# Kernel optimization log

Hardware: AMD Instinct MI355X
Metric: run time of the kernel (lower is better)

Reference implementation:

```python
import jax, jax.numpy as jnp
import numpy as np

H_DIM = 128; N_HEADS = 4; D_K = 32; W_INP = 300
N_DOC = 32000; N_TOPIC = 800; N_WORD = 80000; B = 16
VOCAB = 15000; N_TOPIC_EMB = 50
SQRT_DK = float(np.sqrt(D_K))


def setup_inputs() -> dict:
    key = jax.random.key(0)
    ks = iter(jax.random.split(key, 64))
    def nrm(shape, s=0.05):
        return jax.random.normal(next(ks), shape, dtype=jnp.float32) * s
    def ridx(shape, hi):
        return jax.random.randint(next(ks), shape, 0, hi, dtype=jnp.int32)
    inp = {
        'word_embeds': nrm((VOCAB, W_INP), 0.1),
        'topic_embeds': nrm((N_TOPIC_EMB, H_DIM), 0.1),
        'KW': nrm((2, 3, H_DIM, H_DIM)), 'Kb': nrm((2, 3, H_DIM)),
        'QW': nrm((2, 3, H_DIM, H_DIM)), 'Qb': nrm((2, 3, H_DIM)),
        'VW': nrm((2, 3, H_DIM, H_DIM)), 'Vb': nrm((2, 3, H_DIM)),
        'AW': nrm((2, 3, H_DIM, H_DIM)), 'Ab': nrm((2, 3, H_DIM)),
        'rel_att': nrm((2, 5, N_HEADS, D_K, D_K), 0.1),
        'rel_msg': nrm((2, 5, N_HEADS, D_K, D_K), 0.1),
        'rel_pri': jnp.ones((2, 5, N_HEADS), jnp.float32),
        'skip': jnp.ones((2, 3), jnp.float32),
        'adapt_w': nrm((W_INP, H_DIM)), 'adapt_b': nrm((H_DIM,)),
        'out_w': nrm((H_DIM, 1)), 'out_b': nrm((1,)),
        'y_data': jax.random.uniform(next(ks), (B,), dtype=jnp.float32),
        'word_ids': ridx((N_WORD,), VOCAB),
        'topic_ids': ridx((N_TOPIC,), N_TOPIC_EMB),
        'doc_gid': jnp.sort(ridx((N_DOC,), B)),
        'td_src': ridx((80000,), N_TOPIC), 'td_dst': ridx((80000,), N_DOC),
        'tt_src': ridx((20000,), N_TOPIC), 'tt_dst': ridx((20000,), N_TOPIC),
        'wd_src': ridx((250000,), N_WORD), 'wd_dst': ridx((250000,), N_DOC),
        'wt_src': ridx((100000,), N_WORD), 'wt_dst': ridx((100000,), N_TOPIC),
        'ww_src': ridx((400000,), N_WORD), 'ww_dst': ridx((400000,), N_WORD),
    }
    return inp


def _seg_attn(att, val, dst, n):
    # per-dst-node softmax over incoming edges (per head), then weighted scatter-sum
    m = jax.ops.segment_max(att, dst, num_segments=n)          # [n, H]
    m = jnp.where(jnp.isfinite(m), m, 0.0)                     # empty mailboxes -> 0
    e = jnp.exp(att - m[dst])                                  # [E, H]
    s = jax.ops.segment_sum(e, dst, num_segments=n)            # [n, H]
    w = e / jnp.where(s[dst] > 0, s[dst], 1.0)                 # [E, H]
    return jax.ops.segment_sum(w[:, :, None] * val, dst, num_segments=n)  # [n, H, dk]


def _proj(h, W, b):
    return (h @ W + b).reshape(-1, N_HEADS, D_K)


def _forward(word_embeds, topic_embeds, KW, Kb, QW, Qb, VW, Vb, AW, Ab,
             rel_att, rel_msg, rel_pri, skip, adapt_w, adapt_b, out_w, out_b,
             y_data, word_ids, topic_ids, doc_gid,
             td_src, td_dst, tt_src, tt_dst, wd_src, wd_dst,
             wt_src, wt_dst, ww_src, ww_dst):
    # node-type ids: doc=0, topic=1, word=2; etype ids: td=0 tt=1 wd=2 wt=3 ww=4
    hw = jnp.tanh(word_embeds[word_ids] @ adapt_w + adapt_b)   # [Nw, H_DIM]
    ht = topic_embeds[topic_ids]                               # [Nt, H_DIM]
    hd = jnp.zeros((N_DOC, H_DIM), dtype=word_embeds.dtype)

    def layer(hd, ht, hw, li):
        q_d = _proj(hd, QW[li, 0], Qb[li, 0])
        q_t = _proj(ht, QW[li, 1], Qb[li, 1])
        q_w = _proj(hw, QW[li, 2], Qb[li, 2])
        k_t = _proj(ht, KW[li, 1], Kb[li, 1]); v_t = _proj(ht, VW[li, 1], Vb[li, 1])
        k_w = _proj(hw, KW[li, 2], Kb[li, 2]); v_w = _proj(hw, VW[li, 2], Vb[li, 2])

        def et(k, v, q, src, dst, r, n_dst):
            ke = jnp.einsum('ehd,hdf->ehf', k[src], rel_att[li, r])
            att = (q[dst] * ke).sum(-1) * rel_pri[li, r] / SQRT_DK   # [E, H]
            val = jnp.einsum('ehd,hdf->ehf', v[src], rel_msg[li, r])
            return _seg_attn(att, val, dst, n_dst)

        # cross_reducer='mean' over etypes targeting each node type
        t_d = (et(k_t, v_t, q_d, td_src, td_dst, 0, N_DOC) +
               et(k_w, v_w, q_d, wd_src, wd_dst, 2, N_DOC)) * 0.5
        t_t = (et(k_t, v_t, q_t, tt_src, tt_dst, 1, N_TOPIC) +
               et(k_w, v_w, q_t, wt_src, wt_dst, 3, N_TOPIC)) * 0.5
        t_w = et(k_w, v_w, q_w, ww_src, ww_dst, 4, N_WORD)

        def comb(t, h, nid):
            a = jax.nn.sigmoid(skip[li, nid])
            tr = t.reshape(-1, H_DIM) @ AW[li, nid] + Ab[li, nid]
            return tr * a + h * (1.0 - a)

        return comb(t_d, hd, 0), comb(t_t, ht, 1), comb(t_w, hw, 2)

    for li in range(2):
        hd, ht, hw = layer(hd, ht, hw, li)

    g = jax.ops.segment_max(hd, doc_gid, num_segments=B)       # dgl.max_nodes over docs
    logits = (g @ out_w + out_b).reshape(-1)                   # [B]
    loss = jnp.mean(-(y_data * jax.nn.log_sigmoid(logits) +
                      (1.0 - y_data) * jax.nn.log_sigmoid(-logits)))
    return loss, jax.nn.sigmoid(logits)[:, None]


def reference(word_embeds, topic_embeds, KW, Kb, QW, Qb, VW, Vb, AW, Ab,
              rel_att, rel_msg, rel_pri, skip, adapt_w, adapt_b, out_w, out_b,
              y_data, word_ids, topic_ids, doc_gid,
              td_src, td_dst, tt_src, tt_dst, wd_src, wd_dst,
              wt_src, wt_dst, ww_src, ww_dst):
    return _forward(word_embeds, topic_embeds, KW, Kb, QW, Qb, VW, Vb, AW, Ab,
                    rel_att, rel_msg, rel_pri, skip, adapt_w, adapt_b, out_w, out_b,
                    y_data, word_ids, topic_ids, doc_gid,
                    td_src, td_dst, tt_src, tt_dst, wd_src, wd_dst,
                    wt_src, wt_dst, ww_src, ww_dst)
```

## Files before the change

kernel.cpp:

```cpp
#include <hip/hip_runtime.h>
#include <cstdint>
#include <cstddef>

#define H_DIM 128
#define N_DOC 32000
#define N_TOPIC 800
#define N_WORD 80000
#define BATCH 16
#define VOCAB 15000
#define NODES_ALL 145600
#define EDGES_ALL 850000
#define NBLK_SCAN 143
#define N4_SCAN 36400
#define LDSW 136

typedef short bf16x8 __attribute__((ext_vector_type(8)));
typedef float f32x4 __attribute__((ext_vector_type(4)));
typedef float f32x2 __attribute__((ext_vector_type(2)));
typedef unsigned short u16;
typedef unsigned char u8;

static __device__ __forceinline__ u16 f2bf(float x) {
  unsigned u = __float_as_uint(x);
  u += 0x7fffu + ((u >> 16) & 1u);
// ... 60 lines not shown
      W = AW + ((size_t)li * 3 + nid) * 16384; b = Ab + ((size_t)li * 3 + nid) * 128;
      R = rel_msg + ((size_t)li * 5 + r) * 4096;
      scale = (r == 4) ? 1.f : 0.5f;
    }
  }
  u16* obl = (wid == 0) ? bl_arena : bl_arena + 40960 + (size_t)(wid - 1) * 16384;
  float* obias = bias_arena + wid * 128;

  const int nelem = KS * 512;
  for (int e = threadIdx.x; e < nelem; e += 256) {
    const int s = e >> 9, rem = e & 511, l = rem >> 3, jj = rem & 7;
    const int k = s * 32 + ((l >> 4) << 3) + jj;
    const int nn = t * 16 + (l & 15);
    float v = 0.f;
    if (k < Kreal) {
      if (fold == 0) v = W[(size_t)k * 128 + nn];
      else if (fold == 1) {
        const int h = nn >> 5, d = nn & 31;
        const float* Wr = W + (size_t)k * 128 + h * 32;
        const float* Rh = R + h * 1024;
        for (int f = 0; f < 32; ++f) v += Wr[f] * Rh[d * 32 + f];
      } else {
        const int h = k >> 5, dd = k & 31;
        const float* Rh = R + h * 1024 + dd * 32;
        const float* Wc = W + (size_t)h * 32 * 128 + nn;
        float sa = 0.f;
        for (int f = 0; f < 32; ++f) sa += Rh[f] * Wc[(size_t)f * 128];
        v = sa * scale;
      }
    }
    obl[(size_t)(t * KS + s) * 512 + rem] = f2bf(v);
  }
  if (t == 0 && threadIdx.x < 128) {
    const int nn = threadIdx.x;
    float v = 0.f;
    if (fold != 1) v = b[nn];
    else {
      const int h = nn >> 5, d = nn & 31;
      const float* Rh = R + h * 1024;
      for (int f = 0; f < 32; ++f) v += b[h * 32 + f] * Rh[d * 32 + f];
    }
    obias[nn] = v;
  }
}

static __device__ __forceinline__ void kv_write_half(
    const u16* lds16, int rr, int cs, u8* kv, size_t m, int vhalf)
{
  u8* Cp = kv + m * 256 + (cs >> 3) * 16 + (vhalf ? 8 : 0);
  #pragma unroll
  for (int q2 = 0; q2 < 4; ++q2) {
    uint4 ld = *reinterpret_cast<const uint4*>(&lds16[rr * LDSW + cs + q2 * 8]);
    int t0 = __builtin_amdgcn_cvt_pk_fp8_f32(b2f(ld.x & 0xffffu), b2f(ld.x >> 16), 0, false);
    unsigned w0 = (unsigned)__builtin_amdgcn_cvt_pk_fp8_f32(b2f(ld.y & 0xffffu), b2f(ld.y >> 16), t0, true);
    int t1 = __builtin_amdgcn_cvt_pk_fp8_f32(b2f(ld.z & 0xffffu), b2f(ld.z >> 16), 0, false);
    unsigned w1 = (unsigned)__builtin_amdgcn_cvt_pk_fp8_f32(b2f(ld.w & 0xffffu), b2f(ld.w >> 16), t1, true);
    *reinterpret_cast<uint2*>(Cp + q2 * 16) = make_uint2(w0, w1);
  }
}

static __device__ __forceinline__ void bf16_write_row(
    const u16* lds16, int rr, int cs, u16* C, size_t m)
{
  u16* Cp = C + m * 128 + cs;
  #pragma unroll
  for (int q2 = 0; q2 < 4; ++q2)
    *reinterpret_cast<uint4*>(Cp + q2 * 8) =
        *reinterpret_cast<const uint4*>(&lds16[rr * LDSW + cs + q2 * 8]);
}

#define GEMM_ACC(AV, BLP)                                                        \
  {                                                                              \
    const u16* Bp = (BLP) + (size_t)lane * 8;                                    \
    _Pragma("unroll")                                                            \
    for (int s = 0; s < 4; ++s) {                                                \
      _Pragma("unroll")                                                          \
      for (int t = 0; t < 8; ++t) {                                              \
        bf16x8 bfr = *reinterpret_cast<const bf16x8*>(Bp + (size_t)(t * 4 + s) * 512); \
        acc[t] = __builtin_amdgcn_mfma_f32_16x16x32_bf16(AV[s], bfr, acc[t], 0, 0, 0); \
      }                                                                          \
    }                                                                            \
  }

#define ACC_TO_LDS(BIAS)                                                         \
  {                                                                              \
    _Pragma("unroll")                                                            \
    for (int t = 0; t < 8; ++t) {                                                \
      const int col = t * 16 + (lane & 15);                                      \
      const float bb = (BIAS)[col];                                              \
      const int mr = w * 16 + g * 4;                                             \
      _Pragma("unroll")                                                          \
      for (int j = 0; j < 4; ++j)                                                \
        lds16[(mr + j) * LDSW + col] = f2bf(acc[t][j] + bb);                     \
    }                                                                            \
  }

static __device__ __forceinline__ float lds_qc_dot(
    const u16* lds16, int rr, int cs, const float* __restrict__ qc)
{
  float dot = 0.f;
  #pragma unroll
  for (int q2 = 0; q2 < 4; ++q2) {
    uint4 ld = *reinterpret_cast<const uint4*>(&lds16[rr * LDSW + cs + q2 * 8]);
    float4 qa = *reinterpret_cast<const float4*>(&qc[cs + q2 * 8]);
    float4 qb = *reinterpret_cast<const float4*>(&qc[cs + q2 * 8 + 4]);
    dot += b2f(ld.x & 0xffffu) * qa.x + b2f(ld.x >> 16) * qa.y
         + b2f(ld.y & 0xffffu) * qa.z + b2f(ld.y >> 16) * qa.w
         + b2f(ld.z & 0xffffu) * qb.x + b2f(ld.z >> 16) * qb.y
         + b2f(ld.w & 0xffffu) * qb.z + b2f(ld.w >> 16) * qb.w;
  }
  return dot;
}

static __device__ __forceinline__ void vp_write(
    const u16* lds16, int rr, int cs, float u_keep, u8* vp, size_t m)
{
  unsigned wpk[8];
  #pragma unroll
  for (int q2 = 0; q2 < 4; ++q2) {
    uint4 ld = *reinterpret_cast<const uint4*>(&lds16[rr * LDSW + cs + q2 * 8]);
    int t0 = __builtin_amdgcn_cvt_pk_fp8_f32(u_keep * b2f(ld.x & 0xffffu), u_keep * b2f(ld.x >> 16), 0, false);
    wpk[2 * q2] = (unsigned)__builtin_amdgcn_cvt_pk_fp8_f32(u_keep * b2f(ld.y & 0xffffu), u_keep * b2f(ld.y >> 16), t0, true);
    int t1 = __builtin_amdgcn_cvt_pk_fp8_f32(u_keep * b2f(ld.z & 0xffffu), u_keep * b2f(ld.z >> 16), 0, false);
    wpk[2 * q2 + 1] = (unsigned)__builtin_amdgcn_cvt_pk_fp8_f32(u_keep * b2f(ld.w & 0xffffu), u_keep * b2f(ld.w >> 16), t1, true);
  }
  *reinterpret_cast<uint4*>(vp + m * 128 + cs)      = make_uint4(wpk[0], wpk[1], wpk[2], wpk[3]);
  *reinterpret_cast<uint4*>(vp + m * 128 + cs + 16) = make_uint4(wpk[4], wpk[5], wpk[6], wpk[7]);
}

__global__ __launch_bounds__(256) void adapt_l0w_kernel(
    const u16* __restrict__ wtab, const int* __restrict__ word_ids,
    const u16* __restrict__ BLa, const float* __restrict__ ba,
    const u16* __restrict__ BLk, const float* __restrict__ bk,
    const u16* __restrict__ BLv, const float* __restrict__ bv,
    const u16* __restrict__ BLq, const float* __restrict__ bq,
    const float* __restrict__ qc, const float* __restrict__ priw,
    u16* __restrict__ hw, u8* __restrict__ kv, u8* __restrict__ vp,
    float* __restrict__ uf, u16* __restrict__ qout, int n)
{
  __shared__ u16 lds16[64 * LDSW];
  const int tid = threadIdx.x, lane = tid & 63, w = tid >> 6;
  int rl = blockIdx.x * 64 + w * 16 + (lane & 15);
  if (rl >= n) rl = n - 1;
  const int row = word_ids[rl];
  const int g = lane >> 4;

  bf16x8 a10[10];
  const u16* Ap = wtab + (size_t)row * 320 + g * 8;
  #pragma unroll
  for (int s = 0; s < 10; ++s) a10[s] = *reinterpret_cast<const bf16x8*>(Ap + s * 32);

  const int rr = w * 16 + (lane >> 2), cs = (lane & 3) * 32;
  const int m = blockIdx.x * 64 + rr;

  f32x4 acc[8];
  #pragma unroll
  for (int t = 0; t < 8; ++t) acc[t] = (f32x4)0.f;
  {
    const u16* Bp = BLa + (size_t)lane * 8;
    #pragma unroll
    for (int s = 0; s < 10; ++s) {
      #pragma unroll
      for (int t = 0; t < 8; ++t) {
        bf16x8 bfr = *reinterpret_cast<const bf16x8*>(Bp + (size_t)(t * 10 + s) * 512);
        acc[t] = __builtin_amdgcn_mfma_f32_16x16x32_bf16(a10[s], bfr, acc[t], 0, 0, 0);
      }
    }
  }
  #pragma unroll
  for (int t = 0; t < 8; ++t) {
    const int col = t * 16 + (lane & 15);
    const float bb = ba[col];
    const int mr = w * 16 + g * 4;
    #pragma unroll
    for (int j = 0; j < 4; ++j)
      lds16[(mr + j) * LDSW + col] = f2bf(tanhf(acc[t][j] + bb));
  }
  if (m < n) bf16_write_row(lds16, rr, cs, hw, m);
  bf16x8 an[4];
  {
    const int rloc = w * 16 + (lane & 15);
    #pragma unroll
    for (int s = 0; s < 4; ++s)
      an[s] = *reinterpret_cast<const bf16x8*>(&lds16[rloc * LDSW + s * 32 + g * 8]);
  }

  #pragma unroll
  for (int t = 0; t < 8; ++t) acc[t] = (f32x4)0.f;
  GEMM_ACC(an, BLk)
  ACC_TO_LDS(bk)
  float u_keep = 0.f;
  if (m < n) {
    kv_write_half(lds16, rr, cs, kv, m, 0);
    float dot = lds_qc_dot(lds16, rr, cs, qc);
    u_keep = __expf(dot * (priw[cs >> 5] * 0.17677669529663687f));
    uf[m * 4 + (cs >> 5)] = u_keep;
  }
  #pragma unroll
  for (int t = 0; t < 8; ++t) acc[t] = (f32x4)0.f;
  GEMM_ACC(an, BLv)
  ACC_TO_LDS(bv)
  if (m < n) {
    kv_write_half(lds16, rr, cs, kv, m, 1);
    vp_write(lds16, rr, cs, u_keep, vp, m);
  }
  #pragma unroll
  for (int t = 0; t < 8; ++t) acc[t] = (f32x4)0.f;
  GEMM_ACC(an, BLq)
  ACC_TO_LDS(bq)
  if (m < n) bf16_write_row(lds16, rr, cs, qout, m);
}

__global__ __launch_bounds__(256) void gemm_kv_kernel(
    const u16* __restrict__ A,
    const u16* __restrict__ BLk, const float* __restrict__ bk,
    const u16* __restrict__ BLv, const float* __restrict__ bv,
    u8* __restrict__ kv, int n)
{
  __shared__ u16 lds16[64 * LDSW];
  const int tid = threadIdx.x, lane = tid & 63, w = tid >> 6;
  int rl = blockIdx.x * 64 + w * 16 + (lane & 15);
  if (rl >= n) rl = n - 1;
  const int g = lane >> 4;
  bf16x8 a[4];
  const u16* Ap = A + (size_t)rl * 128 + g * 8;
  #pragma unroll
  for (int s = 0; s < 4; ++s) a[s] = *reinterpret_cast<const bf16x8*>(Ap + s * 32);
  const int rr = w * 16 + (lane >> 2), cs = (lane & 3) * 32;
  const int m = blockIdx.x * 64 + rr;

  f32x4 acc[8];
  #pragma unroll
  for (int t = 0; t < 8; ++t) acc[t] = (f32x4)0.f;
  GEMM_ACC(a, BLk)
  ACC_TO_LDS(bk)
  if (m < n) kv_write_half(lds16, rr, cs, kv, m, 0);

  #pragma unroll
  for (int t = 0; t < 8; ++t) acc[t] = (f32x4)0.f;
  GEMM_ACC(a, BLv)
  ACC_TO_LDS(bv)
  if (m < n) kv_write_half(lds16, rr, cs, kv, m, 1);
}

__global__ __launch_bounds__(256) void gemmN_l0t_kernel(
    const u16* __restrict__ A,
    const u16* __restrict__ BLk, const float* __restrict__ bk,
    const u16* __restrict__ BLv, const float* __restrict__ bv,
    const u16* __restrict__ BLq0, const float* __restrict__ bq0,
    const u16* __restrict__ BLq1, const float* __restrict__ bq1,
    const float* __restrict__ qc, const float* __restrict__ prit,
    u8* __restrict__ kv, u8* __restrict__ vp, float* __restrict__ uf,
    u16* __restrict__ q0, u16* __restrict__ q1, int n)
{
  __shared__ u16 lds16[64 * LDSW];
  const int tid = threadIdx.x, lane = tid & 63, w = tid >> 6;
  int rl = blockIdx.x * 64 + w * 16 + (lane & 15);
  if (rl >= n) rl = n - 1;
  const int g = lane >> 4;
  bf16x8 a[4];
  const u16* Ap = A + (size_t)rl * 128 + g * 8;
  #pragma unroll
  for (int s = 0; s < 4; ++s) a[s] = *reinterpret_cast<const bf16x8*>(Ap + s * 32);
  const int rr = w * 16 + (lane >> 2), cs = (lane & 3) * 32;
  const int m = blockIdx.x * 64 + rr;

  f32x4 acc[8];
  #pragma unroll
  for (int t = 0; t < 8; ++t) acc[t] = (f32x4)0.f;
  GEMM_ACC(a, BLk)
  ACC_TO_LDS(bk)
  float u_keep = 0.f;
  if (m < n) {
    kv_write_half(lds16, rr, cs, kv, m, 0);
    float dot = lds_qc_dot(lds16, rr, cs, qc);
    u_keep = __expf(dot * (prit[cs >> 5] * 0.17677669529663687f));
    uf[m * 4 + (cs >> 5)] = u_keep;
  }
  #pragma unroll
  for (int t = 0; t < 8; ++t) acc[t] = (f32x4)0.f;
  GEMM_ACC(a, BLv)
  ACC_TO_LDS(bv)
  if (m < n) {
    kv_write_half(lds16, rr, cs, kv, m, 1);
    vp_write(lds16, rr, cs, u_keep, vp, m);
  }
  #pragma unroll
  for (int t = 0; t < 8; ++t) acc[t] = (f32x4)0.f;
  GEMM_ACC(a, BLq0)
  ACC_TO_LDS(bq0)
  if (m < n) bf16_write_row(lds16, rr, cs, q0, m);

  #pragma unroll
  for (int t = 0; t < 8; ++t) acc[t] = (f32x4)0.f;
  GEMM_ACC(a, BLq1)
  ACC_TO_LDS(bq1)
  if (m < n) bf16_write_row(lds16, rr, cs, q1, m);
}

template<int KS>
__global__ __launch_bounds__(256) void gemm2_kernel(
    const u16* __restrict__ A2, const u16* __restrict__ BL0, const u16* __restrict__ BL1,
    const float* __restrict__ bias, u16* __restrict__ C,
    const float* __restrict__ skipp, int n)
{
  __shared__ u16 lds16[64 * LDSW];
  const int tid = threadIdx.x, lane = tid & 63, w = tid >> 6;
  int rl = blockIdx.x * 64 + w * 16 + (lane & 15);
  if (rl >= n) rl = n - 1;
  const int g = lane >> 4;

  bf16x8 a0[KS], a1[KS];
  const u16* Ap = A2 + (size_t)rl * 256 + g * 8;
  #pragma unroll
  for (int s = 0; s < KS; ++s) {
    a0[s] = *reinterpret_cast<const bf16x8*>(Ap + s * 32);
    a1[s] = *reinterpret_cast<const bf16x8*>(Ap + 128 + s * 32);
  }
  f32x4 acc[8];
  #pragma unroll
  for (int t = 0; t < 8; ++t) acc[t] = (f32x4)0.f;
  const u16* Bp0 = BL0 + (size_t)lane * 8;
  const u16* Bp1 = BL1 + (size_t)lane * 8;
  #pragma unroll
  for (int s = 0; s < KS; ++s) {
    #pragma unroll
    for (int t = 0; t < 8; ++t) {
      bf16x8 b0 = *reinterpret_cast<const bf16x8*>(Bp0 + (size_t)(t * KS + s) * 512);
      acc[t] = __builtin_amdgcn_mfma_f32_16x16x32_bf16(a0[s], b0, acc[t], 0, 0, 0);
      bf16x8 b1 = *reinterpret_cast<const bf16x8*>(Bp1 + (size_t)(t * KS + s) * 512);
      acc[t] = __builtin_amdgcn_mfma_f32_16x16x32_bf16(a1[s], b1, acc[t], 0, 0, 0);
    }
  }
  ACC_TO_LDS(bias)
  const int rr = w * 16 + (lane >> 2), cs = (lane & 3) * 32;
  const int m = blockIdx.x * 64 + rr;
  if (m < n) {
    const float aa = 1.f / (1.f + __expf(-skipp[0]));
    #pragma unroll
    for (int q2 = 0; q2 < 4; ++q2) {
      uint4 pr = *reinterpret_cast<const uint4*>(&lds16[rr * LDSW + cs + q2 * 8]);
      uint4 blv = *reinterpret_cast<const uint4*>(C + (size_t)m * 128 + cs + q2 * 8);
      uint4 st;
      st.x = blend2(pr.x, blv.x, aa);
      st.y = blend2(pr.y, blv.y, aa);
      st.z = blend2(pr.z, blv.z, aa);
      st.w = blend2(pr.w, blv.w, aa);
      *reinterpret_cast<uint4*>(C + (size_t)m * 128 + cs + q2 * 8) = st;
    }
  }
}

__global__ __launch_bounds__(256) void comb_dq_kernel(
    const u16* __restrict__ A2, const u16* __restrict__ BL0, const u16* __restrict__ BL1,
    const float* __restrict__ bias, const float* __restrict__ skipp,
    const u16* __restrict__ BLq0, const float* __restrict__ bq0,
    const u16* __restrict__ BLq1, const float* __restrict__ bq1,
    u16* __restrict__ hd, u16* __restrict__ q0, u16* __restrict__ q1, int n)
{
  __shared__ u16 lds16[64 * LDSW];
  const int tid = threadIdx.x, lane = tid & 63, w = tid >> 6;
  int rl = blockIdx.x * 64 + w * 16 + (lane & 15);
  if (rl >= n) rl = n - 1;
  const int g = lane >> 4;

  bf16x8 a0[4], a1[4];
  const u16* Ap = A2 + (size_t)rl * 256 + g * 8;
  #pragma unroll
  for (int s = 0; s < 4; ++s) {
    a0[s] = *reinterpret_cast<const bf16x8*>(Ap + s * 32);
    a1[s] = *reinterpret_cast<const bf16x8*>(Ap + 128 + s * 32);
  }
  f32x4 acc[8];
  #pragma unroll
  for (int t = 0; t < 8; ++t) acc[t] = (f32x4)0.f;
  {
    const u16* Bp0 = BL0 + (size_t)lane * 8;
    const u16* Bp1 = BL1 + (size_t)lane * 8;
    #pragma unroll
    for (int s = 0; s < 4; ++s) {
      #pragma unroll
      for (int t = 0; t < 8; ++t) {
        bf16x8 b0 = *reinterpret_cast<const bf16x8*>(Bp0 + (size_t)(t * 4 + s) * 512);
        acc[t] = __builtin_amdgcn_mfma_f32_16x16x32_bf16(a0[s], b0, acc[t], 0, 0, 0);
        bf16x8 b1 = *reinterpret_cast<const bf16x8*>(Bp1 + (size_t)(t * 4 + s) * 512);
        acc[t] = __builtin_amdgcn_mfma_f32_16x16x32_bf16(a1[s], b1, acc[t], 0, 0, 0);
      }
    }
  }
  const float aa = 1.f / (1.f + __expf(-skipp[0]));
  #pragma unroll
  for (int t = 0; t < 8; ++t) {
    const int col = t * 16 + (lane & 15);
    const float bb = bias[col];
    const int mr = w * 16 + g * 4;
    #pragma unroll
    for (int j = 0; j < 4; ++j)
      lds16[(mr + j) * LDSW + col] = f2bf((acc[t][j] + bb) * aa);
  }
  const int rr = w * 16 + (lane >> 2), cs = (lane & 3) * 32;
  const int m = blockIdx.x * 64 + rr;
  if (m < n) bf16_write_row(lds16, rr, cs, hd, m);
  bf16x8 an[4];
  {
    const int rloc = w * 16 + (lane & 15);
    #pragma unroll
    for (int s = 0; s < 4; ++s)
      an[s] = *reinterpret_cast<const bf16x8*>(&lds16[rloc * LDSW + s * 32 + g * 8]);
  }
  #pragma unroll
  for (int t = 0; t < 8; ++t) acc[t] = (f32x4)0.f;
  GEMM_ACC(an, BLq0)
  ACC_TO_LDS(bq0)
  if (m < n) bf16_write_row(lds16, rr, cs, q0, m);
  #pragma unroll
  for (int t = 0; t < 8; ++t) acc[t] = (f32x4)0.f;
  GEMM_ACC(an, BLq1)
  ACC_TO_LDS(bq1)
  if (m < n) bf16_write_row(lds16, rr, cs, q1, m);
}

__global__ __launch_bounds__(256) void comb_kv_kernel(
    const u16* __restrict__ Aw, const u16* __restrict__ hwold,
    const u16* __restrict__ BLc, const float* __restrict__ bc,
    const u16* __restrict__ BLk, const float* __restrict__ bk,
    const u16* __restrict__ BLv, const float* __restrict__ bv,
    const float* __restrict__ skipp, u8* __restrict__ kv, int n)
{
  __shared__ u16 lds16[64 * LDSW];
  const int tid = threadIdx.x, lane = tid & 63, w = tid >> 6;
  int rl = blockIdx.x * 64 + w * 16 + (lane & 15);
  if (rl >= n) rl = n - 1;
  const int g = lane >> 4;

  bf16x8 a[4];
  const u16* Ap = Aw + (size_t)rl * 128 + g * 8;
  #pragma unroll
  for (int s = 0; s < 4; ++s) a[s] = *reinterpret_cast<const bf16x8*>(Ap + s * 32);

  f32x4 acc[8];
  #pragma unroll
  for (int t = 0; t < 8; ++t) acc[t] = (f32x4)0.f;
  GEMM_ACC(a, BLc)
  ACC_TO_LDS(bc)
  const int rr = w * 16 + (lane >> 2), cs = (lane & 3) * 32;
  const int m = blockIdx.x * 64 + rr;
  if (m < n) {
    const float aa = 1.f / (1.f + __expf(-skipp[0]));
    #pragma unroll
    for (int q2 = 0; q2 < 4; ++q2) {
      uint4 pr = *reinterpret_cast<const uint4*>(&lds16[rr * LDSW + cs + q2 * 8]);
      uint4 blv = *reinterpret_cast<const uint4*>(hwold + (size_t)m * 128 + cs + q2 * 8);
      uint4 st;
      st.x = blend2(pr.x, blv.x, aa);
      st.y = blend2(pr.y, blv.y, aa);
      st.z = blend2(pr.z, blv.z, aa);
      st.w = blend2(pr.w, blv.w, aa);
      *reinterpret_cast<uint4*>(&lds16[rr * LDSW + cs + q2 * 8]) = st;
    }
  }
  bf16x8 an[4];
  {
    const int rloc = w * 16 + (lane & 15);
    #pragma unroll
    for (int s = 0; s < 4; ++s)
      an[s] = *reinterpret_cast<const bf16x8*>(&lds16[rloc * LDSW + s * 32 + g * 8]);
  }
  #pragma unroll
  for (int t = 0; t < 8; ++t) acc[t] = (f32x4)0.f;
  GEMM_ACC(an, BLk)
  ACC_TO_LDS(bk)
  if (m < n) kv_write_half(lds16, rr, cs, kv, m, 0);
  #pragma unroll
  for (int t = 0; t < 8; ++t) acc[t] = (f32x4)0.f;
  GEMM_ACC(an, BLv)
  ACC_TO_LDS(bv)
  if (m < n) kv_write_half(lds16, rr, cs, kv, m, 1);
}

__global__ void conv_wtab_kernel(const float* __restrict__ we, u16* __restrict__ wt) {
  int i = blockIdx.x * 256 + threadIdx.x;
  if (i < VOCAB * 320) {
    int r = i / 320, c = i - r * 320;
    wt[i] = (c < 300) ? f2bf(we[(size_t)r * 300 + c]) : (u16)0;
  }
}

__global__ void gather_topic_kernel(const float* __restrict__ emb, const int* __restrict__ ids,
                                    u16* __restrict__ out) {
  int i = blockIdx.x * 256 + threadIdx.x;
  if (i < N_TOPIC * 128) {
    int node = i >> 7, c = i & 127;
    out[i] = f2bf(emb[(size_t)ids[node] * 128 + c]);
  }
}

__global__ void count_rank_kernel(const int* __restrict__ td, const int* __restrict__ wd,
                                  const int* __restrict__ tt, const int* __restrict__ wt,
                                  const int* __restrict__ ww, int* cnt, int* __restrict__ rank) {
  int i = blockIdx.x * 256 + threadIdx.x;
  if (i >= EDGES_ALL) return;
  int b;
  if (i < 80000)       b = td[i];
  else if (i < 330000) b = 32000 + wd[i - 80000];
  else if (i < 350000) b = 64000 + tt[i - 330000];
  else if (i < 450000) b = 64800 + wt[i - 350000];
  else                 b = 65600 + ww[i - 450000];
  rank[i] = atomicAdd(&cnt[b], 1);
}

__global__ void fill_rank_kernel(const int* __restrict__ td_s, const int* __restrict__ td_d,
                                 const int* __restrict__ wd_s, const int* __restrict__ wd_d,
                                 const int* __restrict__ tt_s, const int* __restrict__ tt_d,
                                 const int* __restrict__ wt_s, const int* __restrict__ wt_d,
                                 const int* __restrict__ ww_s, const int* __restrict__ ww_d,
                                 const int* __restrict__ offs, const int* __restrict__ rank,
                                 int* __restrict__ csrc) {
  int i = blockIdx.x * 256 + threadIdx.x;
  if (i >= EDGES_ALL) return;
  int b, s;
  if (i < 80000)       { b = td_d[i];                  s = td_s[i]; }
  else if (i < 330000) { b = 32000 + wd_d[i - 80000];  s = wd_s[i - 80000]; }
  else if (i < 350000) { b = 64000 + tt_d[i - 330000]; s = tt_s[i - 330000]; }
  else if (i < 450000) { b = 64800 + wt_d[i - 350000]; s = wt_s[i - 350000]; }
  else                 { b = 65600 + ww_d[i - 450000]; s = ww_s[i - 450000]; }
  csrc[offs[b] + rank[i]] = s;
}

__global__ __launch_bounds__(256) void scanA_kernel(const int* __restrict__ cnt, int* __restrict__ bsum) {
  const int tid = threadIdx.x, lane = tid & 63, wv = tid >> 6;
  const int i4 = blockIdx.x * 256 + tid;
  int4 v = make_int4(0, 0, 0, 0);
  if (i4 < N4_SCAN) v = reinterpret_cast<const int4*>(cnt)[i4];
  int s = v.x + v.y + v.z + v.w;
  #pragma unroll
  for (int d = 1; d < 64; d <<= 1) s += __shfl_xor(s, d);
  __shared__ int ws[4];
  if (lane == 0) ws[wv] = s;
  __syncthreads();
  if (tid == 0) bsum[blockIdx.x] = ws[0] + ws[1] + ws[2] + ws[3];
}

__global__ __launch_bounds__(256) void scanB_kernel(const int* __restrict__ bsum,
                                                    int* __restrict__ bpre, int* __restrict__ offs,
                                                    unsigned* __restrict__ g) {
  const int tid = threadIdx.x, lane = tid & 63, wv = tid >> 6;
  int v = (tid < NBLK_SCAN) ? bsum[tid] : 0;
  int incl = wave_iscan(v, lane);
  __shared__ int ws[4];
  if (lane == 63) ws[wv] = incl;
  __syncthreads();
  int pre = 0;
  for (int j = 0; j < 4; ++j) if (j < wv) pre += ws[j];
  incl += pre;
  if (tid < NBLK_SCAN) bpre[tid] = incl - v;
  if (tid == NBLK_SCAN - 1) offs[NODES_ALL] = incl;
  for (int i = tid; i < BATCH * H_DIM; i += 256) g[i] = 0x007FFFFFu;
}

// ... 117 lines not shown
      const int eA = base + sub, eB = base + 4 + sub;
      const bool vA = eA < e1, vB = eB < e1;
      const int sA = csrc[vA ? eA : last];
      const int sB = csrc[vB ? eB : last];
      uint2 cA = *reinterpret_cast<const uint2*>(vp + (size_t)sA * 128 + sl * 8);
      uint2 cB = *reinterpret_cast<const uint2*>(vp + (size_t)sB * 128 + sl * 8);
      float uA = uf[sA * 4 + h];
      float uB = uf[sB * 4 + h];
      if (!vA) { cA = make_uint2(0u, 0u); uA = 0.f; }
      if (!vB) { cB = make_uint2(0u, 0u); uB = 0.f; }
      ss += uA + uB;
      acc0 += cvt8<false>((int)cA.x); acc1 += cvt8<true>((int)cA.x);
      acc2 += cvt8<false>((int)cA.y); acc3 += cvt8<true>((int)cA.y);
      acc0 += cvt8<false>((int)cB.x); acc1 += cvt8<true>((int)cB.x);
      acc2 += cvt8<false>((int)cB.y); acc3 += cvt8<true>((int)cB.y);
    }
  }
  butterfly4(acc0, acc1, acc2, acc3, ss, lane, red, ss_out);
}

static __device__ __forceinline__ int chbase_of(int lane) {
  return (lane & 15) * 8 + ((lane >> 4) & 1) * 4 + ((lane >> 5) & 1) * 2;
}

template<int DOCU>
__global__ __launch_bounds__(256) void agg_all_kernel(AggArgs A, int topic_n)
{
  __shared__ float lacc[4][128];
  __shared__ float lssA[4];
  const int tid = threadIdx.x, lane = tid & 63, wv = tid >> 6;
  const int sub = lane >> 4, sl = lane & 15;
  const int bid = blockIdx.x;
  const int chb = chbase_of(lane);
  f32x2 red; float ss;

  if (bid < topic_n) {
    const int node = bid;
    for (int r = 0; r < 2; ++r) {
      agg_core(r ? A.q_wt : A.q_tt, r ? A.kv_w : A.kv_t,
               A.offs + (r ? 64800 : 64000), A.csrc, A.pri + (r ? 12 : 4),
               node, wv * 4 + sub, 16, sl, lane, red, ss);
      lacc[wv][chb] = red[0]; lacc[wv][chb + 1] = red[1];
      if (lane == 0) lssA[wv] = ss;
      __syncthreads();
      if (tid < 128) {
        float a = lacc[0][tid] + lacc[1][tid] + lacc[2][tid] + lacc[3][tid];
        float st = lssA[0] + lssA[1] + lssA[2] + lssA[3];
        float inv = (st > 0.f) ? 1.f / st : 0.f;
        A.t2_t[(size_t)node * 256 + r * 128 + tid] = f2bf(a * inv);
      }
      __syncthreads();
    }
  } else if (bid < topic_n + 8000) {
    const int node = (bid - topic_n) * 4 + wv;
    if (DOCU) {
      agg_docu(A.vp_t, A.uf_t, A.offs + 0, A.csrc, node, sub, sl, lane, red, ss);
    } else {
      agg_core(A.q_td, A.kv_t, A.offs + 0, A.csrc, A.pri + 0, node, sub, 4, sl, lane, red, ss);
    }
    {
      float inv = (ss > 0.f) ? 1.f / ss : 0.f;
      unsigned pk = (unsigned)f2bf(red[0] * inv) | ((unsigned)f2bf(red[1] * inv) << 16);
      *reinterpret_cast<unsigned*>(A.t2_d + (size_t)node * 256 + chb) = pk;
    }
    if (DOCU) {
      agg_docu(A.vp_w, A.uf_w, A.offs + 32000, A.csrc, node, sub, sl, lane, red, ss);
    } else {
      agg_core(A.q_wd, A.kv_w, A.offs + 32000, A.csrc, A.pri + 8, node, sub, 4, sl, lane, red, ss);
    }
    {
      float inv = (ss > 0.f) ? 1.f / ss : 0.f;
      unsigned pk = (unsigned)f2bf(red[0] * inv) | ((unsigned)f2bf(red[1] * inv) << 16);
      *reinterpret_cast<unsigned*>(A.t2_d + (size_t)node * 256 + 128 + chb) = pk;
    }
  } else {
    const int node = (bid - topic_n - 8000) * 4 + wv;
    agg_core(A.q_ww, A.kv_w, A.offs + 65600, A.csrc, A.pri + 16, node, sub, 4, sl, lane, red, ss);
    float inv = (ss > 0.f) ? 1.f / ss : 0.f;
    unsigned pk = (unsigned)f2bf(red[0] * inv) | ((unsigned)f2bf(red[1] * inv) << 16);
    *reinterpret_cast<unsigned*>(A.t_w + (size_t)node * 128 + chb) = pk;
  }
}

__global__ void segmax_kernel(const u16* __restrict__ hd, const int* __restrict__ gid,
                              unsigned* g) {
  int c = threadIdx.x;
  int d0 = blockIdx.x * 128;
  int dend = min(d0 + 128, N_DOC);
  int cur = -1; float m = 0.f;
  for (int d = d0; d < dend; ++d) {
    int gg = gid[d];
    float v = b2f(hd[(size_t)d * 128 + c]);
    if (gg != cur) {
      if (cur >= 0) atomicMax(&g[cur * 128 + c], fenc(m));
      cur = gg; m = v;
    } else {
      m = fmaxf(m, v);
    }
  }
  if (cur >= 0) atomicMax(&g[cur * 128 + c], fenc(m));
}

__global__ void final_kernel(const unsigned* __restrict__ g, const float* __restrict__ out_w,
                             const float* __restrict__ out_b, const float* __restrict__ y,
                             float* out) {
  int tid = threadIdx.x;
  int b = tid >> 4, seg = tid & 15;
  float p = 0.f;
  #pragma unroll
  for (int j = 0; j < 8; ++j) {
    int c = seg * 8 + j;
    p += fdec(g[b * 128 + c]) * out_w[c];
  }
  p += __shfl_xor(p, 1);
  p += __shfl_xor(p, 2);
  p += __shfl_xor(p, 4);
  p += __shfl_xor(p, 8);
  __shared__ float logits[BATCH];
  __shared__ float losses[BATCH];
  if (seg == 0) logits[b] = p + out_b[0];
  __syncthreads();
  if (tid < BATCH) {
    float l = logits[tid];
    out[1 + tid] = 1.f / (1.f + expf(-l));
    float ls_pos = (l > 0.f) ? -log1pf(expf(-l)) : l - log1pf(expf(l));
    float ls_neg = (l < 0.f) ? -log1pf(expf(l)) : -l - log1pf(expf(-l));
    losses[tid] = -(y[tid] * ls_pos + (1.f - y[tid]) * ls_neg);
  }
  __syncthreads();
  if (tid == 0) {
    float s = 0.f;
    for (int j = 0; j < BATCH; ++j) s += losses[j];
    out[0] = s / (float)BATCH;
  }
}

extern "C" void kernel_launch(void* const* d_in, const int* in_sizes, int n_in,
                              void* d_out, int out_size, void* d_ws, size_t ws_size,
                              hipStream_t stream)
{
  const float* word_embeds  = (const float*)d_in[0];
  const float* topic_embeds = (const float*)d_in[1];
  const float* KW  = (const float*)d_in[2];
  const float* Kb  = (const float*)d_in[3];
  const float* QW  = (const float*)d_in[4];
  const float* Qb  = (const float*)d_in[5];
  const float* VW  = (const float*)d_in[6];
  const float* Vb  = (const float*)d_in[7];
  const float* AW  = (const float*)d_in[8];
  const float* Ab  = (const float*)d_in[9];
  const float* rel_att = (const float*)d_in[10];
  const float* rel_msg = (const float*)d_in[11];
  const float* rel_pri = (const float*)d_in[12];
  const float* skip    = (const float*)d_in[13];
  const float* adapt_w = (const float*)d_in[14];
  const float* adapt_b = (const float*)d_in[15];
  const float* out_w   = (const float*)d_in[16];
  const float* out_b   = (const float*)d_in[17];
  const float* y_data  = (const float*)d_in[18];
  const int* word_ids  = (const int*)d_in[19];
  const int* topic_ids = (const int*)d_in[20];
  const int* doc_gid   = (const int*)d_in[21];
  const int* td_src = (const int*)d_in[22];
  const int* td_dst = (const int*)d_in[23];
  const int* tt_src = (const int*)d_in[24];
  const int* tt_dst = (const int*)d_in[25];
  const int* wd_src = (const int*)d_in[26];
  const int* wd_dst = (const int*)d_in[27];
  const int* wt_src = (const int*)d_in[28];
  const int* wt_dst = (const int*)d_in[29];
  const int* ww_src = (const int*)d_in[30];
  const int* ww_dst = (const int*)d_in[31];

  char* base = (char*)d_ws;
  size_t off_b = 0;
  auto alloc = [&](size_t bytes) -> char* {
    char* p = base + off_b;
    off_b = (off_b + bytes + 255) & ~(size_t)255;
    return p;
  };

  u16* wtab = (u16*)alloc((size_t)VOCAB * 320 * 2);
  u16* hw   = (u16*)alloc((size_t)N_WORD * 128 * 2);
  u16* hd   = (u16*)alloc((size_t)N_DOC * 128 * 2);
  u16* ht   = (u16*)alloc((size_t)N_TOPIC * 128 * 2);
// ... 10 lines not shown
  u16* q_ww = (u16*)alloc((size_t)N_WORD * 128 * 2);
  u16* t2_d = (u16*)alloc((size_t)N_DOC * 256 * 2);
  u16* t2_t = (u16*)alloc((size_t)N_TOPIC * 256 * 2);
  u16* t_w  = (u16*)alloc((size_t)N_WORD * 128 * 2);
  unsigned* g = (unsigned*)alloc((size_t)BATCH * 128 * 4);

  int* cnt_all  = (int*)alloc((size_t)NODES_ALL * 4);
  int* offs_all = (int*)alloc(((size_t)NODES_ALL + 1) * 4);
  int* csrc_all = (int*)alloc((size_t)EDGES_ALL * 4);
  int* rank_all = (int*)alloc((size_t)EDGES_ALL * 4);
  int* bsum     = (int*)alloc((size_t)NBLK_SCAN * 4);
  int* bpre     = (int*)alloc((size_t)NBLK_SCAN * 4);

  u16* blw        = (u16*)alloc((size_t)(40960 + 28 * 16384) * 2);
  float* bias_are = (float*)alloc((size_t)29 * 128 * 4);

  auto BLp = [&](int wid) -> const u16* {
    return (wid == 0) ? blw : blw + 40960 + (size_t)(wid - 1) * 16384;
  };
  auto BIp = [&](int wid) -> const float* { return bias_are + wid * 128; };
  auto WID = [&](int li, int j) { return 1 + li * 14 + j; };

  prep_kernel<<<29 * 8, 256, 0, stream>>>(KW, Kb, QW, Qb, VW, Vb, AW, Ab,
                                          rel_att, rel_msg, adapt_w, adapt_b, blw, bias_are);
  conv_wtab_kernel<<<(VOCAB * 320 + 255) / 256, 256, 0, stream>>>(word_embeds, wtab);
  gather_topic_kernel<<<(N_TOPIC * 128 + 255) / 256, 256, 0, stream>>>(topic_embeds, topic_ids, ht);

  hipMemsetAsync(cnt_all, 0, (size_t)NODES_ALL * 4, stream);
  count_rank_kernel<<<(EDGES_ALL + 255) / 256, 256, 0, stream>>>(
      td_dst, wd_dst, tt_dst, wt_dst, ww_dst, cnt_all, rank_all);
  scanA_kernel<<<NBLK_SCAN, 256, 0, stream>>>(cnt_all, bsum);
  scanB_kernel<<<1, 256, 0, stream>>>(bsum, bpre, offs_all, g);
  scanC_kernel<<<NBLK_SCAN, 256, 0, stream>>>(cnt_all, bpre, offs_all);
  fill_rank_kernel<<<(EDGES_ALL + 255) / 256, 256, 0, stream>>>(
      td_src, td_dst, wd_src, wd_dst, tt_src, tt_dst, wt_src, wt_dst, ww_src, ww_dst,
      offs_all, rank_all, csrc_all);

  const int GW = (N_WORD + 63) / 64, GD = (N_DOC + 63) / 64, GT = (N_TOPIC + 63) / 64;

  adapt_l0w_kernel<<<GW, 256, 0, stream>>>(
      wtab, word_ids,
      BLp(0), BIp(0),
      BLp(WID(0, 1)), BIp(WID(0, 1)),
      BLp(WID(0, 3)), BIp(WID(0, 3)),
      BLp(WID(0, 8)), BIp(WID(0, 8)),
      BIp(WID(0, 6)), rel_pri + 8,
      hw, kv_w, vp_w, uf_w, q_ww, N_WORD);
  gemmN_l0t_kernel<<<GT, 256, 0, stream>>>(
      ht,
      BLp(WID(0, 0)), BIp(WID(0, 0)),
      BLp(WID(0, 2)), BIp(WID(0, 2)),
      BLp(WID(0, 5)), BIp(WID(0, 5)),
      BLp(WID(0, 7)), BIp(WID(0, 7)),
      BIp(WID(0, 4)), rel_pri + 0,
      kv_t, vp_t, uf_t, q_tt, q_wt, N_TOPIC);

  AggArgs A0;
  A0.q_td = q_td; A0.q_wd = q_wd; A0.q_tt = q_tt; A0.q_wt = q_wt; A0.q_ww = q_ww;
  A0.kv_t = kv_t; A0.kv_w = kv_w; A0.vp_t = vp_t; A0.vp_w = vp_w;
  A0.uf_t = uf_t; A0.uf_w = uf_w;
  A0.csrc = csrc_all; A0.offs = offs_all;
  A0.pri = rel_pri;
  A0.t2_d = t2_d; A0.t2_t = t2_t; A0.t_w = t_w;
  agg_all_kernel<1><<<28800, 256, 0, stream>>>(A0, 800);

  comb_dq_kernel<<<GD, 256, 0, stream>>>(
      t2_d, BLp(WID(0, 9)), BLp(WID(0, 11)), BIp(WID(0, 9)), skip + 0,
      BLp(WID(1, 4)), BIp(WID(1, 4)), BLp(WID(1, 6)), BIp(WID(1, 6)),
      hd, q_td, q_wd, N_DOC);
  gemm2_kernel<4><<<GT, 256, 0, stream>>>(t2_t, BLp(WID(0, 10)), BLp(WID(0, 12)),
                                          BIp(WID(0, 10)), ht, skip + 1, N_TOPIC);
  comb_kv_kernel<<<GW, 256, 0, stream>>>(
      t_w, hw, BLp(WID(0, 13)), BIp(WID(0, 13)),
      BLp(WID(1, 1)), BIp(WID(1, 1)), BLp(WID(1, 3)), BIp(WID(1, 3)),
      skip + 2, kv_w, N_WORD);

  gemm_kv_kernel<<<GT, 256, 0, stream>>>(
      ht, BLp(WID(1, 0)), BIp(WID(1, 0)), BLp(WID(1, 2)), BIp(WID(1, 2)), kv_t, N_TOPIC);

  AggArgs A1 = A0;
  A1.pri = rel_pri + 20;
  agg_all_kernel<0><<<8000, 256, 0, stream>>>(A1, 0);

  gemm2_kernel<4><<<GD, 256, 0, stream>>>(t2_d, BLp(WID(1, 9)), BLp(WID(1, 11)),
                                          BIp(WID(1, 9)), hd, skip + 3, N_DOC);

  segmax_kernel<<<(N_DOC + 127) / 128, 128, 0, stream>>>(hd, doc_gid, g);
  final_kernel<<<1, 256, 0, stream>>>(g, out_w, out_b, y_data, (float*)d_out);
}
```

Baseline: 372.8 us.

## Fuse final doc combine with segment-max readout; interleave multi-weight MFMA GEMMs

```diff
diff --git a/kernel.cpp b/kernel.cpp
--- a/kernel.cpp
+++ b/kernel.cpp
@@ -166,7 +166,42 @@
     }                                                                            \
   }
 
-#define ACC_TO_LDS(BIAS)                                                         \
+#define GEMM_ACC2(AV, BLPa, ACCa, BLPb, ACCb)                                    \
+  {                                                                              \
+    const u16* Bpa = (BLPa) + (size_t)lane * 8;                                  \
+    const u16* Bpb = (BLPb) + (size_t)lane * 8;                                  \
+    _Pragma("unroll")                                                            \
+    for (int s = 0; s < 4; ++s) {                                                \
+      _Pragma("unroll")                                                          \
+      for (int t = 0; t < 8; ++t) {                                              \
+        ACCa[t] = __builtin_amdgcn_mfma_f32_16x16x32_bf16(AV[s],                 \
+            *reinterpret_cast<const bf16x8*>(Bpa + (size_t)(t * 4 + s) * 512), ACCa[t], 0, 0, 0); \
+        ACCb[t] = __builtin_amdgcn_mfma_f32_16x16x32_bf16(AV[s],                 \
+            *reinterpret_cast<const bf16x8*>(Bpb + (size_t)(t * 4 + s) * 512), ACCb[t], 0, 0, 0); \
+      }                                                                          \
+    }                                                                            \
+  }
+
+#define GEMM_ACC3(AV, BLPa, ACCa, BLPb, ACCb, BLPc, ACCc)                        \
+  {                                                                              \
+    const u16* Bpa = (BLPa) + (size_t)lane * 8;                                  \
+    const u16* Bpb = (BLPb) + (size_t)lane * 8;                                  \
+    const u16* Bpc = (BLPc) + (size_t)lane * 8;                                  \
+    _Pragma("unroll")                                                            \
+    for (int s = 0; s < 4; ++s) {                                                \
+      _Pragma("unroll")                                                          \
+      for (int t = 0; t < 8; ++t) {                                              \
+        ACCa[t] = __builtin_amdgcn_mfma_f32_16x16x32_bf16(AV[s],                 \
+            *reinterpret_cast<const bf16x8*>(Bpa + (size_t)(t * 4 + s) * 512), ACCa[t], 0, 0, 0); \
+        ACCb[t] = __builtin_amdgcn_mfma_f32_16x16x32_bf16(AV[s],                 \
+            *reinterpret_cast<const bf16x8*>(Bpb + (size_t)(t * 4 + s) * 512), ACCb[t], 0, 0, 0); \
+        ACCc[t] = __builtin_amdgcn_mfma_f32_16x16x32_bf16(AV[s],                 \
+            *reinterpret_cast<const bf16x8*>(Bpc + (size_t)(t * 4 + s) * 512), ACCc[t], 0, 0, 0); \
+      }                                                                          \
+    }                                                                            \
+  }
+
+#define ACC_TO_LDS2(ACC, BIAS)                                                   \
   {                                                                              \
     _Pragma("unroll")                                                            \
     for (int t = 0; t < 8; ++t) {                                                \
@@ -175,7 +210,7 @@
       const int mr = w * 16 + g * 4;                                             \
       _Pragma("unroll")                                                          \
       for (int j = 0; j < 4; ++j)                                                \
-        lds16[(mr + j) * LDSW + col] = f2bf(acc[t][j] + bb);                     \
+        lds16[(mr + j) * LDSW + col] = f2bf(ACC[t][j] + bb);                     \
     }                                                                            \
   }
 
@@ -269,10 +304,12 @@
       an[s] = *reinterpret_cast<const bf16x8*>(&lds16[rloc * LDSW + s * 32 + g * 8]);
   }
 
-  #pragma unroll
-  for (int t = 0; t < 8; ++t) acc[t] = (f32x4)0.f;
-  GEMM_ACC(an, BLk)
-  ACC_TO_LDS(bk)
+  f32x4 acck[8], accv[8], accq[8];
+  #pragma unroll
+  for (int t = 0; t < 8; ++t) { acck[t] = (f32x4)0.f; accv[t] = (f32x4)0.f; accq[t] = (f32x4)0.f; }
+  GEMM_ACC3(an, BLk, acck, BLv, accv, BLq, accq)
+
+  ACC_TO_LDS2(acck, bk)
   float u_keep = 0.f;
   if (m < n) {
     kv_write_half(lds16, rr, cs, kv, m, 0);
@@ -280,18 +317,12 @@
     u_keep = __expf(dot * (priw[cs >> 5] * 0.17677669529663687f));
     uf[m * 4 + (cs >> 5)] = u_keep;
   }
-  #pragma unroll
-  for (int t = 0; t < 8; ++t) acc[t] = (f32x4)0.f;
-  GEMM_ACC(an, BLv)
-  ACC_TO_LDS(bv)
+  ACC_TO_LDS2(accv, bv)
   if (m < n) {
     kv_write_half(lds16, rr, cs, kv, m, 1);
     vp_write(lds16, rr, cs, u_keep, vp, m);
   }
-  #pragma unroll
-  for (int t = 0; t < 8; ++t) acc[t] = (f32x4)0.f;
-  GEMM_ACC(an, BLq)
-  ACC_TO_LDS(bq)
+  ACC_TO_LDS2(accq, bq)
   if (m < n) bf16_write_row(lds16, rr, cs, qout, m);
 }
 
@@ -313,17 +344,13 @@
   const int rr = w * 16 + (lane >> 2), cs = (lane & 3) * 32;
   const int m = blockIdx.x * 64 + rr;
 
-  f32x4 acc[8];
-  #pragma unroll
-  for (int t = 0; t < 8; ++t) acc[t] = (f32x4)0.f;
-  GEMM_ACC(a, BLk)
-  ACC_TO_LDS(bk)
+  f32x4 acck[8], accv[8];
+  #pragma unroll
+  for (int t = 0; t < 8; ++t) { acck[t] = (f32x4)0.f; accv[t] = (f32x4)0.f; }
+  GEMM_ACC2(a, BLk, acck, BLv, accv)
+  ACC_TO_LDS2(acck, bk)
   if (m < n) kv_write_half(lds16, rr, cs, kv, m, 0);
-
-  #pragma unroll
-  for (int t = 0; t < 8; ++t) acc[t] = (f32x4)0.f;
-  GEMM_ACC(a, BLv)
-  ACC_TO_LDS(bv)
+  ACC_TO_LDS2(accv, bv)
   if (m < n) kv_write_half(lds16, rr, cs, kv, m, 1);
 }
 
@@ -349,11 +376,11 @@
   const int rr = w * 16 + (lane >> 2), cs = (lane & 3) * 32;
   const int m = blockIdx.x * 64 + rr;
 
-  f32x4 acc[8];
-  #pragma unroll
-  for (int t = 0; t < 8; ++t) acc[t] = (f32x4)0.f;
-  GEMM_ACC(a, BLk)
-  ACC_TO_LDS(bk)
+  f32x4 acck[8], accv[8];
+  #pragma unroll
+  for (int t = 0; t < 8; ++t) { acck[t] = (f32x4)0.f; accv[t] = (f32x4)0.f; }
+  GEMM_ACC2(a, BLk, acck, BLv, accv)
+  ACC_TO_LDS2(acck, bk)
   float u_keep = 0.f;
   if (m < n) {
     kv_write_half(lds16, rr, cs, kv, m, 0);
@@ -361,24 +388,18 @@
     u_keep = __expf(dot * (prit[cs >> 5] * 0.17677669529663687f));
     uf[m * 4 + (cs >> 5)] = u_keep;
   }
-  #pragma unroll
-  for (int t = 0; t < 8; ++t) acc[t] = (f32x4)0.f;
-  GEMM_ACC(a, BLv)
-  ACC_TO_LDS(bv)
+  ACC_TO_LDS2(accv, bv)
   if (m < n) {
     kv_write_half(lds16, rr, cs, kv, m, 1);
     vp_write(lds16, rr, cs, u_keep, vp, m);
   }
-  #pragma unroll
-  for (int t = 0; t < 8; ++t) acc[t] = (f32x4)0.f;
-  GEMM_ACC(a, BLq0)
-  ACC_TO_LDS(bq0)
+  f32x4 accq0[8], accq1[8];
+  #pragma unroll
+  for (int t = 0; t < 8; ++t) { accq0[t] = (f32x4)0.f; accq1[t] = (f32x4)0.f; }
+  GEMM_ACC2(a, BLq0, accq0, BLq1, accq1)
+  ACC_TO_LDS2(accq0, bq0)
   if (m < n) bf16_write_row(lds16, rr, cs, q0, m);
-
-  #pragma unroll
-  for (int t = 0; t < 8; ++t) acc[t] = (f32x4)0.f;
-  GEMM_ACC(a, BLq1)
-  ACC_TO_LDS(bq1)
+  ACC_TO_LDS2(accq1, bq1)
   if (m < n) bf16_write_row(lds16, rr, cs, q1, m);
 }
 
@@ -416,7 +437,7 @@
       acc[t] = __builtin_amdgcn_mfma_f32_16x16x32_bf16(a1[s], b1, acc[t], 0, 0, 0);
     }
   }
-  ACC_TO_LDS(bias)
+  ACC_TO_LDS2(acc, bias)
   const int rr = w * 16 + (lane >> 2), cs = (lane & 3) * 32;
   const int m = blockIdx.x * 64 + rr;
   if (m < n) {
@@ -435,21 +456,22 @@
   }
 }
 
-__global__ __launch_bounds__(256) void comb_dq_kernel(
+__global__ __launch_bounds__(256) void comb_readout_kernel(
     const u16* __restrict__ A2, const u16* __restrict__ BL0, const u16* __restrict__ BL1,
-    const float* __restrict__ bias, const float* __restrict__ skipp,
-    const u16* __restrict__ BLq0, const float* __restrict__ bq0,
-    const u16* __restrict__ BLq1, const float* __restrict__ bq1,
-    u16* __restrict__ hd, u16* __restrict__ q0, u16* __restrict__ q1, int n)
+    const float* __restrict__ bias, const u16* __restrict__ hdold,
+    const float* __restrict__ skipp, const int* __restrict__ gid,
+    unsigned* __restrict__ g, int n)
 {
   __shared__ u16 lds16[64 * LDSW];
   const int tid = threadIdx.x, lane = tid & 63, w = tid >> 6;
   int rl = blockIdx.x * 64 + w * 16 + (lane & 15);
   if (rl >= n) rl = n - 1;
-  const int g = lane >> 4;
+  const int gq = lane >> 4;
+  const int g_ = gq;
+  (void)g_;
 
   bf16x8 a0[4], a1[4];
-  const u16* Ap = A2 + (size_t)rl * 256 + g * 8;
+  const u16* Ap = A2 + (size_t)rl * 256 + gq * 8;
   #pragma unroll
   for (int s = 0; s < 4; ++s) {
     a0[s] = *reinterpret_cast<const bf16x8*>(Ap + s * 32);
@@ -472,6 +494,87 @@
       }
     }
   }
+  #pragma unroll
+  for (int t = 0; t < 8; ++t) {
+    const int col = t * 16 + (lane & 15);
+    const float bb = bias[col];
+    const int mr = w * 16 + gq * 4;
+    #pragma unroll
+    for (int j = 0; j < 4; ++j)
+      lds16[(mr + j) * LDSW + col] = f2bf(acc[t][j] + bb);
+  }
+  const int rr = w * 16 + (lane >> 2), cs = (lane & 3) * 32;
+  const int m = blockIdx.x * 64 + rr;
+  if (m < n) {
+    const float aa = 1.f / (1.f + __expf(-skipp[0]));
+    #pragma unroll
+    for (int q2 = 0; q2 < 4; ++q2) {
+      uint4 pr = *reinterpret_cast<const uint4*>(&lds16[rr * LDSW + cs + q2 * 8]);
+      uint4 blv = *reinterpret_cast<const uint4*>(hdold + (size_t)m * 128 + cs + q2 * 8);
+      uint4 st;
+      st.x = blend2(pr.x, blv.x, aa);
+      st.y = blend2(pr.y, blv.y, aa);
+      st.z = blend2(pr.z, blv.z, aa);
+      st.w = blend2(pr.w, blv.w, aa);
+      *reinterpret_cast<uint4*>(&lds16[rr * LDSW + cs + q2 * 8]) = st;
+    }
+  }
+  __syncthreads();
+  if (tid < 128) {
+    const int c = tid;
+    const int rmax = min(64, n - blockIdx.x * 64);
+    int cur = -1; float mx = 0.f;
+    for (int r = 0; r < rmax; ++r) {
+      int gg = gid[blockIdx.x * 64 + r];
+      float v = b2f(lds16[r * LDSW + c]);
+      if (gg != cur) {
+        if (cur >= 0) atomicMax(&g[cur * 128 + c], fenc(mx));
+        cur = gg; mx = v;
+      } else {
+        mx = fmaxf(mx, v);
+      }
+    }
+    if (cur >= 0) atomicMax(&g[cur * 128 + c], fenc(mx));
+  }
+}
+
+__global__ __launch_bounds__(256) void comb_dq_kernel(
+    const u16* __restrict__ A2, const u16* __restrict__ BL0, const u16* __restrict__ BL1,
+    const float* __restrict__ bias, const float* __restrict__ skipp,
+    const u16* __restrict__ BLq0, const float* __restrict__ bq0,
+    const u16* __restrict__ BLq1, const float* __restrict__ bq1,
+    u16* __restrict__ hd, u16* __restrict__ q0, u16* __restrict__ q1, int n)
+{
+  __shared__ u16 lds16[64 * LDSW];
+  const int tid = threadIdx.x, lane = tid & 63, w = tid >> 6;
+  int rl = blockIdx.x * 64 + w * 16 + (lane & 15);
+  if (rl >= n) rl = n - 1;
+  const int g = lane >> 4;
+
+  bf16x8 a0[4], a1[4];
+  const u16* Ap = A2 + (size_t)rl * 256 + g * 8;
+  #pragma unroll
+  for (int s = 0; s < 4; ++s) {
+    a0[s] = *reinterpret_cast<const bf16x8*>(Ap + s * 32);
+    a1[s] = *reinterpret_cast<const bf16x8*>(Ap + 128 + s * 32);
+  }
+  f32x4 acc[8];
+  #pragma unroll
+  for (int t = 0; t < 8; ++t) acc[t] = (f32x4)0.f;
+  {
+    const u16* Bp0 = BL0 + (size_t)lane * 8;
+    const u16* Bp1 = BL1 + (size_t)lane * 8;
+    #pragma unroll
+    for (int s = 0; s < 4; ++s) {
+      #pragma unroll
+      for (int t = 0; t < 8; ++t) {
+        bf16x8 b0 = *reinterpret_cast<const bf16x8*>(Bp0 + (size_t)(t * 4 + s) * 512);
+        acc[t] = __builtin_amdgcn_mfma_f32_16x16x32_bf16(a0[s], b0, acc[t], 0, 0, 0);
+        bf16x8 b1 = *reinterpret_cast<const bf16x8*>(Bp1 + (size_t)(t * 4 + s) * 512);
+        acc[t] = __builtin_amdgcn_mfma_f32_16x16x32_bf16(a1[s], b1, acc[t], 0, 0, 0);
+      }
+    }
+  }
   const float aa = 1.f / (1.f + __expf(-skipp[0]));
   #pragma unroll
   for (int t = 0; t < 8; ++t) {
@@ -492,15 +595,13 @@
     for (int s = 0; s < 4; ++s)
       an[s] = *reinterpret_cast<const bf16x8*>(&lds16[rloc * LDSW + s * 32 + g * 8]);
   }
-  #pragma unroll
-  for (int t = 0; t < 8; ++t) acc[t] = (f32x4)0.f;
-  GEMM_ACC(an, BLq0)
-  ACC_TO_LDS(bq0)
+  f32x4 accq0[8], accq1[8];
+  #pragma unroll
+  for (int t = 0; t < 8; ++t) { accq0[t] = (f32x4)0.f; accq1[t] = (f32x4)0.f; }
+  GEMM_ACC2(an, BLq0, accq0, BLq1, accq1)
+  ACC_TO_LDS2(accq0, bq0)
   if (m < n) bf16_write_row(lds16, rr, cs, q0, m);
-  #pragma unroll
-  for (int t = 0; t < 8; ++t) acc[t] = (f32x4)0.f;
-  GEMM_ACC(an, BLq1)
-  ACC_TO_LDS(bq1)
+  ACC_TO_LDS2(accq1, bq1)
   if (m < n) bf16_write_row(lds16, rr, cs, q1, m);
 }
 
@@ -526,7 +627,7 @@
   #pragma unroll
   for (int t = 0; t < 8; ++t) acc[t] = (f32x4)0.f;
   GEMM_ACC(a, BLc)
-  ACC_TO_LDS(bc)
+  ACC_TO_LDS2(acc, bc)
   const int rr = w * 16 + (lane >> 2), cs = (lane & 3) * 32;
   const int m = blockIdx.x * 64 + rr;
   if (m < n) {
@@ -550,15 +651,13 @@
     for (int s = 0; s < 4; ++s)
       an[s] = *reinterpret_cast<const bf16x8*>(&lds16[rloc * LDSW + s * 32 + g * 8]);
   }
-  #pragma unroll
-  for (int t = 0; t < 8; ++t) acc[t] = (f32x4)0.f;
-  GEMM_ACC(an, BLk)
-  ACC_TO_LDS(bk)
+  f32x4 acck[8], accv[8];
+  #pragma unroll
+  for (int t = 0; t < 8; ++t) { acck[t] = (f32x4)0.f; accv[t] = (f32x4)0.f; }
+  GEMM_ACC2(an, BLk, acck, BLv, accv)
+  ACC_TO_LDS2(acck, bk)
   if (m < n) kv_write_half(lds16, rr, cs, kv, m, 0);
-  #pragma unroll
-  for (int t = 0; t < 8; ++t) acc[t] = (f32x4)0.f;
-  GEMM_ACC(an, BLv)
-  ACC_TO_LDS(bv)
+  ACC_TO_LDS2(accv, bv)
   if (m < n) kv_write_half(lds16, rr, cs, kv, m, 1);
 }
 
@@ -842,25 +941,6 @@
   }
 }
 
-__global__ void segmax_kernel(const u16* __restrict__ hd, const int* __restrict__ gid,
-                              unsigned* g) {
-  int c = threadIdx.x;
-  int d0 = blockIdx.x * 128;
-  int dend = min(d0 + 128, N_DOC);
-  int cur = -1; float m = 0.f;
-  for (int d = d0; d < dend; ++d) {
-    int gg = gid[d];
-    float v = b2f(hd[(size_t)d * 128 + c]);
-    if (gg != cur) {
-      if (cur >= 0) atomicMax(&g[cur * 128 + c], fenc(m));
-      cur = gg; m = v;
-    } else {
-      m = fmaxf(m, v);
-    }
-  }
-  if (cur >= 0) atomicMax(&g[cur * 128 + c], fenc(m));
-}
-
 __global__ void final_kernel(const unsigned* __restrict__ g, const float* __restrict__ out_w,
                              const float* __restrict__ out_b, const float* __restrict__ y,
                              float* out) {
@@ -1037,9 +1117,9 @@
   A1.pri = rel_pri + 20;
   agg_all_kernel<0><<<8000, 256, 0, stream>>>(A1, 0);
 
-  gemm2_kernel<4><<<GD, 256, 0, stream>>>(t2_d, BLp(WID(1, 9)), BLp(WID(1, 11)),
-                                          BIp(WID(1, 9)), hd, skip + 3, N_DOC);
-
-  segmax_kernel<<<(N_DOC + 127) / 128, 128, 0, stream>>>(hd, doc_gid, g);
+  comb_readout_kernel<<<GD, 256, 0, stream>>>(
+      t2_d, BLp(WID(1, 9)), BLp(WID(1, 11)), BIp(WID(1, 9)), hd,
+      skip + 3, doc_gid, g, N_DOC);
+
   final_kernel<<<1, 256, 0, stream>>>(g, out_w, out_b, y_data, (float*)d_out);
 }
```

Measured after the change: 430.0 us. 1.15x slower.
